# Kernel optimization log

Hardware: AMD Instinct MI355X
Metric: run time of the kernel (lower is better)

Reference implementation:

```python
import jax, jax.numpy as jnp
import numpy as np

B, C, H, W = 4, 16, 512, 512


def setup_inputs() -> dict:
    key = jax.random.key(0)
    k1, k2, k3, k4, k5 = jax.random.split(key, 5)
    # positive depth in [0.5, 10.5] meters
    depth = jax.random.uniform(k1, (B, 1, H, W), dtype=jnp.float32) * 10.0 + 0.5
    # realistic, well-conditioned camera intrinsics per batch element
    fx = 500.0 + 20.0 * jax.random.normal(k2, (B,), dtype=jnp.float32)
    fy = 500.0 + 20.0 * jax.random.normal(k3, (B,), dtype=jnp.float32)
    zeros = jnp.zeros((B,), jnp.float32)
    ones = jnp.ones((B,), jnp.float32)
    K = jnp.stack([
        jnp.stack([fx, zeros, ones * (W / 2.0)], axis=-1),
        jnp.stack([zeros, fy, ones * (H / 2.0)], axis=-1),
        jnp.stack([zeros, zeros, ones], axis=-1),
    ], axis=1)  # [B,3,3]
    # near-identity rigid-ish transforms so homogeneous w ~ 1
    T = jnp.eye(4, dtype=jnp.float32)[None, None] + 0.05 * jax.random.normal(k4, (B, C, 4, 4), dtype=jnp.float32)
    masks = jax.random.randint(k5, (B, C, H, W), 0, 2).astype(jnp.bool_)
    return {"depth": depth, "K": K, "T": T, "masks": masks}


def reference(depth, K, T, masks):
    b, _, h, w = depth.shape
    c = masks.shape[1]
    n = h * w
    eps = 1e-10
    # --- depth -> point cloud ---
    u = jnp.arange(w, dtype=depth.dtype)
    v = jnp.arange(h, dtype=depth.dtype)
    uu, vv = jnp.meshgrid(u, v, indexing='xy')            # [H,W]
    uv1 = jnp.stack([uu, vv, jnp.ones_like(uu)], axis=-1)  # [H,W,3]
    K_inv = jnp.linalg.inv(K)                              # [B,3,3]
    d = jnp.transpose(depth, (0, 2, 3, 1))                 # [B,H,W,1]
    points_3d = jnp.einsum('bij,hwj->bhwi', K_inv, uv1) * d  # [B,H,W,3]
    # --- per-object masked transform (vectorized over all channels) ---
    pts = points_3d.reshape(b, n, 3)
    pts_h = jnp.concatenate([pts, jnp.ones((b, n, 1), pts.dtype)], axis=-1)  # [B,N,4]
    trans_h = jnp.einsum('bcij,bnj->bcni', T, pts_h)       # [B,C,N,4]
    trans3 = trans_h[..., :3] / (trans_h[..., 3:] + eps)   # [B,C,N,3]
    masks_flat = masks.reshape(b, c, n)
    out = pts
    for ci in range(c):
        out = jnp.where(masks_flat[:, ci, :, None], trans3[:, ci], out)
    tp = out.reshape(b, h, w, 3)                           # transformed points
    # --- reproject to depth map (scatter) ---
    p2h = jnp.einsum('bij,bhwj->bhwi', K, tp)              # [B,H,W,3]
    p2 = p2h[..., :2] / (p2h[..., 2:] + eps)
    Z = tp[..., 2]                                         # [B,H,W]
    u_idx = jnp.clip(p2[..., 0], 0, w - 1).astype(jnp.int32)
    v_idx = jnp.clip(p2[..., 1], 0, h - 1).astype(jnp.int32)
    b_idx = jnp.broadcast_to(jnp.arange(b)[:, None, None], (b, h, w))
    depth_map = depth.at[b_idx, 0, v_idx, u_idx].set(Z)
    return depth_map
```

## Files before the change

### kernel.cpp

```cpp
#include <hip/hip_runtime.h>
#include <stdint.h>

constexpr int B = 4, C = 16, H = 512, W = 512;
constexpr int N = H * W;
constexpr int BLOCKS_PER_BATCH = N / 256;
constexpr float EPS = 1e-10f;


__global__ __launch_bounds__(256) void project_store_kernel(
    const float* __restrict__ depth,
    const float* __restrict__ K,
    const float* __restrict__ T,
    const int*   __restrict__ masks,
    unsigned long long* __restrict__ keys,
    unsigned* __restrict__ tbuf,
    float*    __restrict__ zbuf)
{
    __shared__ float Ts[16][17];

    int b = blockIdx.x >> 10;
    int n = ((blockIdx.x & (BLOCKS_PER_BATCH - 1)) << 8) + threadIdx.x;
    int idx = b * N + n;
    int v = n >> 9;
    int u = n & (W - 1);

    {
        int t = threadIdx.x;
        int c = t >> 4, e = t & 15;
        Ts[e][c] = T[(size_t)b * 256 + t];
    }
    __syncthreads();

    float d = depth[idx];

    const float* Kb = K + b * 9;
    float k00 = Kb[0], k01 = Kb[1], k02 = Kb[2];
    float k10 = Kb[3], k11 = Kb[4], k12 = Kb[5];
    float k20 = Kb[6], k21 = Kb[7], k22 = Kb[8];

    float c00 =  (k11 * k22 - k12 * k21);
    float c01 = -(k10 * k22 - k12 * k20);
    float c02 =  (k10 * k21 - k11 * k20);
    float det = k00 * c00 + k01 * c01 + k02 * c02;
    float invdet = 1.0f / det;
    float i00 =  (k11 * k22 - k12 * k21) * invdet;
    float i01 = -(k01 * k22 - k02 * k21) * invdet;
    float i02 =  (k01 * k12 - k02 * k11) * invdet;
    float i10 = -(k10 * k22 - k12 * k20) * invdet;
    float i11 =  (k00 * k22 - k02 * k20) * invdet;
    float i12 = -(k00 * k12 - k02 * k10) * invdet;
    float i20 =  (k10 * k21 - k11 * k20) * invdet;
    float i21 = -(k00 * k21 - k01 * k20) * invdet;
    float i22 =  (k00 * k11 - k01 * k10) * invdet;

    float uf = (float)u, vf = (float)v;
    float px = (i00 * uf + i01 * vf + i02) * d;
    float py = (i10 * uf + i11 * vf + i12) * d;
    float pz = (i20 * uf + i21 * vf + i22) * d;

    const int* mb = masks + (size_t)b * C * N + n;
    int sel = -1;
    {
        int m[8];
        #pragma unroll
        for (int c = 0; c < 8; ++c) m[c] = mb[(size_t)(8 + c) * N];
        #pragma unroll
        for (int c = 7; c >= 0; --c) { if (m[c] != 0) { sel = 8 + c; break; } }
        if (sel < 0) {
            #pragma unroll
            for (int c = 0; c < 8; ++c) m[c] = mb[(size_t)c * N];
            #pragma unroll
            for (int c = 7; c >= 0; --c) { if (m[c] != 0) { sel = c; break; } }
        }
    }

    float ox = px, oy = py, oz = pz;
    if (sel >= 0) {
        float tx = Ts[0][sel]  * px + Ts[1][sel]  * py + Ts[2][sel]  * pz + Ts[3][sel];
        float ty = Ts[4][sel]  * px + Ts[5][sel]  * py + Ts[6][sel]  * pz + Ts[7][sel];
        float tz = Ts[8][sel]  * px + Ts[9][sel]  * py + Ts[10][sel] * pz + Ts[11][sel];
        float tw = Ts[12][sel] * px + Ts[13][sel] * py + Ts[14][sel] * pz + Ts[15][sel];
        float denom = tw + EPS;
        ox = tx / denom;
        oy = ty / denom;
        oz = tz / denom;
    }

    float qx = k00 * ox + k01 * oy + k02 * oz;
    float qy = k10 * ox + k11 * oy + k12 * oz;
    float qz = k20 * ox + k21 * oy + k22 * oz;
    float zz = qz + EPS;
    float pu = qx / zz;
    float pv = qy / zz;
    pu = fminf(fmaxf(pu, 0.0f), (float)(W - 1));
    pv = fminf(fmaxf(pv, 0.0f), (float)(H - 1));
    int ui = (int)pu;
    int vi = (int)pv;
    unsigned t = (unsigned)(vi * W + ui);

    unsigned long long key =
        ((unsigned long long)(unsigned)n << 32) |
        (unsigned long long)__float_as_uint(oz);

    tbuf[idx] = t;
    zbuf[idx] = oz;
    keys[(size_t)b * N + t] = key;
}

__global__ __launch_bounds__(256) void fixup_kernel(
    unsigned long long* __restrict__ keys,
    const unsigned* __restrict__ tbuf,
    const float*    __restrict__ zbuf)
{
    int b = blockIdx.x >> 10;
    int n = ((blockIdx.x & (BLOCKS_PER_BATCH - 1)) << 8) + threadIdx.x;
    int idx = b * N + n;
    unsigned t = tbuf[idx];
    float z = zbuf[idx];
    unsigned long long* cell = &keys[(size_t)b * N + t];
    unsigned hi = (unsigned)(*cell >> 32);
    if (hi > (unsigned)(N - 1) || hi < (unsigned)n) {
        unsigned long long key =
            ((unsigned long long)(unsigned)n << 32) |
            (unsigned long long)__float_as_uint(z);
        atomicMax(cell, key);
    }
}

__global__ __launch_bounds__(256) void resolve_kernel(
    const unsigned long long* __restrict__ keys,
    const float*              __restrict__ depth,
    float*                    __restrict__ out)
{
    int idx = blockIdx.x * blockDim.x + threadIdx.x;
    if (idx >= B * N) return;
    unsigned long long k = keys[idx];
    unsigned hi = (unsigned)(k >> 32);
    out[idx] = (hi <= (unsigned)(N - 1)) ? __uint_as_float((unsigned)k)
                                         : depth[idx];
}

extern "C" void kernel_launch(void* const* d_in, const int* in_sizes, int n_in,
                              void* d_out, int out_size, void* d_ws, size_t ws_size,
                              hipStream_t stream) {
    const float* depth = (const float*)d_in[0];
    const float* K     = (const float*)d_in[1];
    const float* T     = (const float*)d_in[2];
    const int*   masks = (const int*)d_in[3];
    float* out = (float*)d_out;

    char* ws = (char*)d_ws;
    unsigned long long* keys = (unsigned long long*)ws;
    unsigned* tbuf = (unsigned*)(ws + (size_t)B * N * 8);
    float*    zbuf = (float*)(ws + (size_t)B * N * 12);

    int grid = B * BLOCKS_PER_BATCH;
    project_store_kernel<<<grid, 256, 0, stream>>>(depth, K, T, masks, keys, tbuf, zbuf);
    fixup_kernel<<<grid, 256, 0, stream>>>(keys, tbuf, zbuf);
    resolve_kernel<<<grid, 256, 0, stream>>>(keys, depth, out);
}
```

Before: 135.1 us.

## Pack target and depth into one record, shrink mask probe groups, skip dominated fixups

The projection kernel now writes the target cell and depth bits as a single 64-bit record instead of two separate arrays, so the fixup kernel does one load per pixel. Mask loads are split into four groups of four channels instead of two groups of eight, cutting speculative mask traffic for pixels whose highest set channel is high. The fixup kernel also uses wave shuffles to drop pixels when a later lane within four positions targets the same cell, avoiding redundant reads and atomics. The trade-off is more serialized load latency in the mask search and a little shuffle overhead.

```diff
diff --git a/kernel.cpp b/kernel.cpp
--- a/kernel.cpp
+++ b/kernel.cpp
@@ -13,8 +13,7 @@
     const float* __restrict__ T,
     const int*   __restrict__ masks,
     unsigned long long* __restrict__ keys,
-    unsigned* __restrict__ tbuf,
-    float*    __restrict__ zbuf)
+    unsigned long long* __restrict__ recs)
 {
     __shared__ float Ts[16][17];
 
@@ -59,18 +58,25 @@
     float pz = (i20 * uf + i21 * vf + i22) * d;
 
     const int* mb = masks + (size_t)b * C * N + n;
-    int sel = -1;
+    int sel;
     {
-        int m[8];
-        #pragma unroll
-        for (int c = 0; c < 8; ++c) m[c] = mb[(size_t)(8 + c) * N];
-        #pragma unroll
-        for (int c = 7; c >= 0; --c) { if (m[c] != 0) { sel = 8 + c; break; } }
+        int m3 = mb[(size_t)15 * N], m2 = mb[(size_t)14 * N];
+        int m1 = mb[(size_t)13 * N], m0 = mb[(size_t)12 * N];
+        sel = m3 ? 15 : m2 ? 14 : m1 ? 13 : m0 ? 12 : -1;
         if (sel < 0) {
-            #pragma unroll
-            for (int c = 0; c < 8; ++c) m[c] = mb[(size_t)c * N];
-            #pragma unroll
-            for (int c = 7; c >= 0; --c) { if (m[c] != 0) { sel = c; break; } }
+            m3 = mb[(size_t)11 * N]; m2 = mb[(size_t)10 * N];
+            m1 = mb[(size_t)9 * N];  m0 = mb[(size_t)8 * N];
+            sel = m3 ? 11 : m2 ? 10 : m1 ? 9 : m0 ? 8 : -1;
+        }
+        if (sel < 0) {
+            m3 = mb[(size_t)7 * N]; m2 = mb[(size_t)6 * N];
+            m1 = mb[(size_t)5 * N]; m0 = mb[(size_t)4 * N];
+            sel = m3 ? 7 : m2 ? 6 : m1 ? 5 : m0 ? 4 : -1;
+        }
+        if (sel < 0) {
+            m3 = mb[(size_t)3 * N]; m2 = mb[(size_t)2 * N];
+            m1 = mb[(size_t)1 * N]; m0 = mb[0];
+            sel = m3 ? 3 : m2 ? 2 : m1 ? 1 : m0 ? 0 : -1;
         }
     }
 
@@ -97,32 +103,39 @@
     int ui = (int)pu;
     int vi = (int)pv;
     unsigned t = (unsigned)(vi * W + ui);
+    unsigned zbits = __float_as_uint(oz);
 
-    unsigned long long key =
-        ((unsigned long long)(unsigned)n << 32) |
-        (unsigned long long)__float_as_uint(oz);
-
-    tbuf[idx] = t;
-    zbuf[idx] = oz;
-    keys[(size_t)b * N + t] = key;
+    recs[idx] = ((unsigned long long)t << 32) | (unsigned long long)zbits;
+    keys[(size_t)b * N + t] =
+        ((unsigned long long)(unsigned)n << 32) | (unsigned long long)zbits;
 }
 
 __global__ __launch_bounds__(256) void fixup_kernel(
     unsigned long long* __restrict__ keys,
-    const unsigned* __restrict__ tbuf,
-    const float*    __restrict__ zbuf)
+    const unsigned long long* __restrict__ recs)
 {
     int b = blockIdx.x >> 10;
     int n = ((blockIdx.x & (BLOCKS_PER_BATCH - 1)) << 8) + threadIdx.x;
     int idx = b * N + n;
-    unsigned t = tbuf[idx];
-    float z = zbuf[idx];
+    int lane = threadIdx.x & 63;
+
+    unsigned long long rec = recs[idx];
+    unsigned t = (unsigned)(rec >> 32);
+    unsigned zbits = (unsigned)rec;
+
+    bool dom = false;
+    #pragma unroll
+    for (int delta = 1; delta <= 4; ++delta) {
+        unsigned tn = (unsigned)__shfl_down((int)t, delta);
+        dom |= (lane + delta < 64) && (tn == t);
+    }
+    if (dom) return;
+
     unsigned long long* cell = &keys[(size_t)b * N + t];
     unsigned hi = (unsigned)(*cell >> 32);
     if (hi > (unsigned)(N - 1) || hi < (unsigned)n) {
         unsigned long long key =
-            ((unsigned long long)(unsigned)n << 32) |
-            (unsigned long long)__float_as_uint(z);
+            ((unsigned long long)(unsigned)n << 32) | (unsigned long long)zbits;
         atomicMax(cell, key);
     }
 }
@@ -151,11 +164,10 @@
 
     char* ws = (char*)d_ws;
     unsigned long long* keys = (unsigned long long*)ws;
-    unsigned* tbuf = (unsigned*)(ws + (size_t)B * N * 8);
-    float*    zbuf = (float*)(ws + (size_t)B * N * 12);
+    unsigned long long* recs = (unsigned long long*)(ws + (size_t)B * N * 8);
 
     int grid = B * BLOCKS_PER_BATCH;
-    project_store_kernel<<<grid, 256, 0, stream>>>(depth, K, T, masks, keys, tbuf, zbuf);
-    fixup_kernel<<<grid, 256, 0, stream>>>(keys, tbuf, zbuf);
+    project_store_kernel<<<grid, 256, 0, stream>>>(depth, K, T, masks, keys, recs);
+    fixup_kernel<<<grid, 256, 0, stream>>>(keys, recs);
     resolve_kernel<<<grid, 256, 0, stream>>>(keys, depth, out);
 }
```

Result: no change. 133.5 us (-1.2%).
